# Performance work log

Hardware: AMD Instinct MI355X
Metric: run time of the kernel (lower is better)

## Reference

```python
import jax, jax.numpy as jnp
import numpy as np

V, B, T, D, H = 32000, 64, 256, 512, 1024


def setup_inputs() -> dict:
    key = jax.random.key(0)
    ks = jax.random.split(key, 8)
    s = lambda i, shape: (jax.random.normal(ks[i], shape, jnp.float32) * 0.02)
    return {
        "y": jax.random.randint(ks[0], (B, T), 0, V),
        "hidden": jnp.zeros((B, H), jnp.float32),
        "emb_table": s(1, (V, D)),
        "Wx": s(2, (D, 3 * H)),
        "Wh": s(3, (H, 3 * H)),
        "bx": jnp.zeros((3 * H,), jnp.float32),
        "bh": jnp.zeros((3 * H,), jnp.float32),
        "W_out": s(4, (H, D)),
        "b_out": jnp.zeros((D,), jnp.float32),
    }


def _gru_step(h, x, Wx, Wh, bx, bh):
    # PyTorch GRUCell semantics: r,z gates, candidate n with r gating the
    # recurrent contribution (including its bias term).
    gx = x @ Wx + bx          # [B, 3H]
    gh = h @ Wh + bh          # [B, 3H]
    xr, xz, xn = jnp.split(gx, 3, axis=-1)
    hr, hz, hn = jnp.split(gh, 3, axis=-1)
    r = jax.nn.sigmoid(xr + hr)
    z = jax.nn.sigmoid(xz + hz)
    n = jnp.tanh(xn + r * hn)
    return (1.0 - z) * n + z * h


def reference(y, hidden, emb_table, Wx, Wh, bx, bh, W_out, b_out):
    emb = emb_table[y]                       # [B, T, D] token embedding lookup

    def step(h, x_t):                        # x_t: [B, D]
        h2 = _gru_step(h, x_t, Wx, Wh, bx, bh)
        return h2, h2

    _, outs = jax.lax.scan(step, hidden, jnp.swapaxes(emb, 0, 1))  # [T, B, H]
    out = jnp.swapaxes(outs, 0, 1)           # [B, T, H] decoder hiddens
    logits = jnp.tanh(out @ W_out + b_out)   # [B, T, D]; dropout_rate=0 -> identity
    return logits
```

## Files before the change

kernel.cpp:

```cpp
#include <hip/hip_runtime.h>
#include <stdint.h>

typedef unsigned short u16;
typedef unsigned int u32;
typedef __attribute__((ext_vector_type(4))) unsigned int u32x4;
typedef __attribute__((ext_vector_type(4))) float f32x4;
typedef __attribute__((ext_vector_type(8))) __bf16 bf16x8;

#define MFMA16(a, b, c) __builtin_amdgcn_mfma_f32_16x16x32_bf16((a), (b), (c), 0, 0, 0)

__device__ __forceinline__ u16 f2b(float f) {
  union { float f; unsigned u; } v; v.f = f;
  unsigned r = v.u + 0x7FFFu + ((v.u >> 16) & 1u);
  return (u16)(r >> 16);
}
__device__ __forceinline__ float b2f(u16 h) {
  union { unsigned u; float f; } v; v.u = ((unsigned)h) << 16;
  return v.f;
}
__device__ __forceinline__ float sigm(float x) { return 1.0f / (1.0f + __expf(-x)); }
__device__ __forceinline__ float tanh_fast(float x) {
  x = fminf(fmaxf(x, -15.0f), 15.0f);
  float t = __expf(2.0f * x);
  return (t - 1.0f) / (t + 1.0f);
}

__device__ __forceinline__ void st16_sc(void* p, u32x4 v) {
  asm volatile("global_store_dwordx4 %0, %1, off sc0 sc1"
               :: "v"(p), "v"(v) : "memory");
}
__device__ __forceinline__ void st4_sc(u32* p, u32 v) {
  asm volatile("global_store_dword %0, %1, off sc0 sc1"
               :: "v"(p), "v"(v) : "memory");
}


__global__ void transpose_cvt(const float* __restrict__ src, u16* __restrict__ dst,
                              int R, int C) {
  __shared__ float tile[32][33];
  const int c0 = blockIdx.x * 32, r0 = blockIdx.y * 32;
  const int tx = threadIdx.x, ty = threadIdx.y;
  for (int i = ty; i < 32; i += 8)
    tile[i][tx] = src[(size_t)(r0 + i) * C + (c0 + tx)];
  __syncthreads();
  for (int i = ty; i < 32; i += 8)
    dst[(size_t)(c0 + i) * R + (r0 + tx)] = f2b(tile[tx][i]);
}

__global__ void gather_cast(const int* __restrict__ y, const float* __restrict__ tab,
                            u16* __restrict__ A) {
  const int idx = blockIdx.x * 256 + threadIdx.x;
  const int m = idx >> 7;
  const int d0 = (idx & 127) << 2;
  const float4 v = *reinterpret_cast<const float4*>(tab + (size_t)y[m] * 512 + d0);
  ushort4 o;
  o.x = f2b(v.x); o.y = f2b(v.y); o.z = f2b(v.z); o.w = f2b(v.w);
  *reinterpret_cast<ushort4*>(A + (size_t)m * 512 + d0) = o;
}

__global__ void cast_h0_blocked(const float* __restrict__ h, u16* __restrict__ dst) {
  const int i = blockIdx.x * 256 + threadIdx.x;
  const int b = i >> 10, n = i & 1023;
  const int r = b >> 4, ii = b & 15, g = n >> 4, j = n & 15;
  dst[((size_t)r * 64 + g) * 256 + ii * 16 + j] = f2b(h[(size_t)b * 1024 + n]);
}

template <int EPI, int ALAYOUT>
__global__ __launch_bounds__(256, 2) void gemm_bt(
    const u16* __restrict__ A, const u16* __restrict__ Bt,
    const float* __restrict__ bias, void* __restrict__ Cout,
    int M, int N, int K) {
  __shared__ u16 As[4096], Bs[4096];
  const int tid = threadIdx.x, lane = tid & 63, w = tid >> 6;
  const int wm = w >> 1, wn = w & 1, c = lane & 15, hq = lane >> 4;
  const int m0 = blockIdx.y * 128, n0 = blockIdx.x * 128;
  f32x4 acc[4][4] = {};

  const int slot0 = tid, slot1 = 256 + tid;
  const int r0_ = slot0 >> 2, ko0 = (slot0 & 3) << 3;
  const int r1_ = slot1 >> 2, ko1 = (slot1 & 3) << 3;

  for (int k0 = 0; k0 < K; k0 += 32) {
    u32x4 a0, a1;
    if (ALAYOUT == 0) {
      a0 = *(const u32x4*)(A + (size_t)(m0 + r0_) * K + k0 + ko0);
      a1 = *(const u32x4*)(A + (size_t)(m0 + r1_) * K + k0 + ko1);
    } else {
      const int ma = m0 + r0_, ka = k0 + ko0, mb = m0 + r1_, kb = k0 + ko1;
      a0 = *(const u32x4*)(A + ((((size_t)(ma >> 6) + 1) * 4 + ((ma >> 4) & 3)) * 64 +
                                (ka >> 4)) * 256 + (ma & 15) * 16 + (ka & 15));
      a1 = *(const u32x4*)(A + ((((size_t)(mb >> 6) + 1) * 4 + ((mb >> 4) & 3)) * 64 +
                                (kb >> 4)) * 256 + (mb & 15) * 16 + (kb & 15));
    }
    const u32x4 b0 = *(const u32x4*)(Bt + (size_t)(n0 + r0_) * K + k0 + ko0);
    const u32x4 b1 = *(const u32x4*)(Bt + (size_t)(n0 + r1_) * K + k0 + ko1);
    __syncthreads();
    *(u32x4*)(As + r0_ * 32 + ko0) = a0;
    *(u32x4*)(As + r1_ * 32 + ko1) = a1;
    *(u32x4*)(Bs + r0_ * 32 + ko0) = b0;
    *(u32x4*)(Bs + r1_ * 32 + ko1) = b1;
    __syncthreads();
    u32x4 af[4], bf[4];
#pragma unroll
    for (int i = 0; i < 4; ++i) {
      af[i] = *(const u32x4*)(As + (wm * 64 + i * 16 + c) * 32 + hq * 8);
      bf[i] = *(const u32x4*)(Bs + (wn * 64 + i * 16 + c) * 32 + hq * 8);
    }
#pragma unroll
    for (int mi = 0; mi < 4; ++mi)
#pragma unroll
      for (int ni = 0; ni < 4; ++ni)
        acc[mi][ni] = MFMA16(__builtin_bit_cast(bf16x8, af[mi]),
                             __builtin_bit_cast(bf16x8, bf[ni]), acc[mi][ni]);
  }

#pragma unroll
  for (int ni = 0; ni < 4; ++ni) {
    const int col = n0 + wn * 64 + ni * 16 + c;
    const float bv = bias[col];
#pragma unroll
    for (int mi = 0; mi < 4; ++mi) {
#pragma unroll
      for (int i = 0; i < 4; ++i) {
        const int m = m0 + wm * 64 + mi * 16 + hq * 4 + i;
        const float v = acc[mi][ni][i] + bv;
        if (EPI == 0) {
          const int dr = (m & 255) * 64 + (m >> 8);
          ((u16*)Cout)[(size_t)dr * N + col] = f2b(v);
        } else {
          const int dr = (m & 63) * 256 + (m >> 6);
          ((float*)Cout)[(size_t)dr * N + col] = tanh_fast(v);
        }
      }
    }
  }
}

__global__ __launch_bounds__(320, 1) void scan_kernel(
    const u16* __restrict__ wh_t,
    const float* __restrict__ bh,
    const float* __restrict__ h0,
    const u16* __restrict__ gx,
    u16* __restrict__ hbuf,
    u32* __restrict__ tags) {
  __shared__ u16 whs[96 * 512];
  __shared__ float red[2][4][3][256];
  __shared__ __align__(16) u16 htile[16][16];
  const int g = blockIdx.x >> 2, r = blockIdx.x & 3;
  const int tid = threadIdx.x, lane = tid & 63, s = tid >> 6;
  const int c = lane & 15, hq = lane >> 4;
  const int gcol = g * 16 + c;
  const int row0 = r * 16;

  for (int fb = s; fb < 96; fb += 5) {
    const int ss = fb / 24, kk = (fb % 24) / 3, ct = fb % 3;
    const int n = ct * 1024 + g * 16 + c;
    const int k = ss * 256 + kk * 32 + hq * 8;
    *(u32x4*)(whs + fb * 512 + lane * 8) =
        *(const u32x4*)(wh_t + (size_t)n * 1024 + k);
  }
  float bhv[3], hprev[4];
  u16 gxr[4][3];
  if (s == 4) {
#pragma unroll
    for (int ct = 0; ct < 3; ++ct) bhv[ct] = bh[ct * 1024 + gcol];
#pragma unroll
    for (int i = 0; i < 4; ++i)
      hprev[i] = h0[(size_t)(row0 + hq * 4 + i) * 1024 + gcol];
    const u16* gp = gx + gcol;
#pragma unroll
    for (int i = 0; i < 4; ++i) {
      const int b = row0 + hq * 4 + i;
      gxr[i][0] = gp[(size_t)b * 3072];
      gxr[i][1] = gp[(size_t)b * 3072 + 1024];
      gxr[i][2] = gp[(size_t)b * 3072 + 2048];
    }
  }
  __syncthreads();

  for (int t = 0; t < 256; ++t) {
    if (s < 4) {
      if (t > 0) {
        const u32* tp = tags + ((size_t)(t & 1) * 4 + r) * (64 * 32) +
                        (s * 16 + (lane & 15)) * 32;
        u32 v0, v1;
        asm volatile("global_load_dword %0, %1, off sc0 sc1" : "=v"(v0) : "v"(tp));
        asm volatile("global_load_dword %0, %1, off sc0 sc1" : "=v"(v1) : "v"(tp));
        while (true) {
          asm volatile("s_waitcnt vmcnt(1)" ::: "memory");
          if (!__ballot(v0 < (u32)t)) break;
          asm volatile("global_load_dword %0, %1, off sc0 sc1" : "=v"(v0) : "v"(tp));
          asm volatile("s_waitcnt vmcnt(1)" ::: "memory");
          if (!__ballot(v1 < (u32)t)) break;
          asm volatile("global_load_dword %0, %1, off sc0 sc1" : "=v"(v1) : "v"(tp));
        }
        asm volatile("s_waitcnt vmcnt(0)" ::: "memory");
      }

      u32x4 af[8];
      {
        const u16* ap0 = hbuf + ((size_t)t * 4 + r) * 16384 +
                         (s * 16 + (hq >> 1)) * 256 + c * 16 + (hq & 1) * 8;
        const u16* ap1 = ap0 + 2048;
        af[0] = *(const u32x4*)(ap0);
        af[1] = *(const u32x4*)(ap0 + 512);
        af[2] = *(const u32x4*)(ap0 + 1024);
        af[3] = *(const u32x4*)(ap0 + 1536);
        af[4] = *(const u32x4*)(ap1);
        af[5] = *(const u32x4*)(ap1 + 512);
        af[6] = *(const u32x4*)(ap1 + 1024);
        af[7] = *(const u32x4*)(ap1 + 1536);
      }

      f32x4 acc[3] = {};
#pragma unroll
      for (int kk = 0; kk < 8; ++kk) {
        const int fb = (s * 8 + kk) * 3;
        const u32x4 b0 = *(const u32x4*)(whs + (fb + 0) * 512 + lane * 8);
        const u32x4 b1 = *(const u32x4*)(whs + (fb + 1) * 512 + lane * 8);
        const u32x4 b2 = *(const u32x4*)(whs + (fb + 2) * 512 + lane * 8);
        const bf16x8 a = __builtin_bit_cast(bf16x8, af[kk]);
        acc[0] = MFMA16(a, __builtin_bit_cast(bf16x8, b0), acc[0]);
        acc[1] = MFMA16(a, __builtin_bit_cast(bf16x8, b1), acc[1]);
        acc[2] = MFMA16(a, __builtin_bit_cast(bf16x8, b2), acc[2]);
      }
#pragma unroll
      for (int ct = 0; ct < 3; ++ct)
        *(f32x4*)&red[t & 1][s][ct][lane * 4] = acc[ct];
    }
    __syncthreads();

    if (s == 4) {
      f32x4 a0 = {}, a1 = {}, a2 = {};
#pragma unroll
      for (int j = 0; j < 4; ++j) {
        a0 += *(const f32x4*)&red[t & 1][j][0][lane * 4];
        a1 += *(const f32x4*)&red[t & 1][j][1][lane * 4];
        a2 += *(const f32x4*)&red[t & 1][j][2][lane * 4];
      }
#pragma unroll
      for (int i = 0; i < 4; ++i) {
        const float xr = b2f(gxr[i][0]);
        const float xz = b2f(gxr[i][1]);
        const float xn = b2f(gxr[i][2]);
        const float rr = sigm(xr + a0[i] + bhv[0]);
        const float zz = sigm(xz + a1[i] + bhv[1]);
        const float nn = tanh_fast(xn + rr * (a2[i] + bhv[2]));
        const float hnew = (1.0f - zz) * nn + zz * hprev[i];
        hprev[i] = hnew;
        htile[hq * 4 + i][c] = f2b(hnew);
      }
      asm volatile("s_waitcnt lgkmcnt(0)" ::: "memory");
      __builtin_amdgcn_sched_barrier(0);
      if (lane < 32) {
        const u32x4 hv = *(const u32x4*)((const u16*)htile + lane * 8);
        st16_sc(hbuf + ((size_t)(t + 1) * 4 + r) * 16384 + g * 256 + lane * 8, hv);
      }
      asm volatile("s_waitcnt vmcnt(0)" ::: "memory");
      if (lane == 0)
        st4_sc(tags + ((size_t)((t + 1) & 1) * 4 + r) * (64 * 32) + g * 32,
               (u32)(t + 1));
      if (t < 255) {
        const u16* gp = gx + (size_t)(t + 1) * 64 * 3072 + gcol;
#pragma unroll
        for (int i = 0; i < 4; ++i) {
          const int b = row0 + hq * 4 + i;
          gxr[i][0] = gp[(size_t)b * 3072];
          gxr[i][1] = gp[(size_t)b * 3072 + 1024];
          gxr[i][2] = gp[(size_t)b * 3072 + 2048];
        }
      }
    }
  }
}

extern "C" void kernel_launch(void* const* d_in, const int* in_sizes, int n_in,
                              void* d_out, int out_size, void* d_ws, size_t ws_size,
                              hipStream_t stream) {
  (void)in_sizes; (void)n_in; (void)out_size; (void)ws_size;
  const int* y = (const int*)d_in[0];
  const float* hidden = (const float*)d_in[1];
  const float* emb = (const float*)d_in[2];
  const float* Wx = (const float*)d_in[3];
  const float* Wh = (const float*)d_in[4];
  const float* bx = (const float*)d_in[5];
  const float* bh = (const float*)d_in[6];
  const float* Wout = (const float*)d_in[7];
  const float* bout = (const float*)d_in[8];

  char* p = (char*)d_ws;
  u16* wx_t = (u16*)p; p += (size_t)3072 * 512 * 2;
  u16* wh_t = (u16*)p; p += (size_t)3072 * 1024 * 2;
  u16* wo_t = (u16*)p; p += (size_t)512 * 1024 * 2;
  u16* aemb = (u16*)p; p += (size_t)16384 * 512 * 2;
  u16* gx   = (u16*)p; p += (size_t)16384 * 3072 * 2;
  u16* hbuf = (u16*)p; p += (size_t)257 * 4 * 64 * 256 * 2;
  u32* tags = (u32*)p;

  hipMemsetAsync(tags, 0, 2 * 4 * 64 * 32 * sizeof(u32), stream);
  transpose_cvt<<<dim3(96, 16), dim3(32, 8), 0, stream>>>(Wx, wx_t, 512, 3072);
  transpose_cvt<<<dim3(96, 32), dim3(32, 8), 0, stream>>>(Wh, wh_t, 1024, 3072);
  transpose_cvt<<<dim3(16, 32), dim3(32, 8), 0, stream>>>(Wout, wo_t, 1024, 512);
  gather_cast<<<dim3(8192), dim3(256), 0, stream>>>(y, emb, aemb);
  cast_h0_blocked<<<dim3(256), dim3(256), 0, stream>>>(hidden, hbuf);

  gemm_bt<0, 0><<<dim3(24, 128), dim3(256), 0, stream>>>(aemb, wx_t, bx, (void*)gx,
                                                         16384, 3072, 512);
  scan_kernel<<<dim3(256), dim3(320), 0, stream>>>(wh_t, bh, hidden, gx,
                                                   hbuf, tags);
  gemm_bt<1, 1><<<dim3(4, 128), dim3(256), 0, stream>>>(hbuf, wo_t, bout,
                                                        d_out, 16384, 512, 1024);
}
```

Measured before the change: 1.057 ms.

## Restructure GRU scan: one block per column group, each wave owns a batch slice

Before, each of 256 blocks (one column group crossed with one batch quarter) split K across four waves and reduced the partial sums in shared memory, with a fifth wave doing the gate math. Now 64 blocks each cover one column group, and each of four waves owns 16 batch rows and does the full K=1024 reduction in registers with 32 MFMA steps. That removes the shared-memory reduction, the __syncthreads and the separate epilogue wave. Hidden-state loads use staged vmcnt waits to overlap the loads with the MFMAs. The cost is 4x fewer blocks and a longer serial MFMA chain per wave each step, and each wave now polls all 64 tags for its batch slice.

```diff
diff --git a/kernel.cpp b/kernel.cpp
--- a/kernel.cpp
+++ b/kernel.cpp
@@ -25,6 +25,13 @@
   return (t - 1.0f) / (t + 1.0f);
 }
 
+template <int OFF>
+__device__ __forceinline__ u32x4 ld16_sc(const void* p) {
+  u32x4 r;
+  asm volatile("global_load_dwordx4 %0, %1, off offset:%2 sc0 sc1"
+               : "=v"(r) : "v"(p), "i"(OFF));
+  return r;
+}
 __device__ __forceinline__ void st16_sc(void* p, u32x4 v) {
   asm volatile("global_store_dwordx4 %0, %1, off sc0 sc1"
                :: "v"(p), "v"(v) : "memory");
@@ -32,6 +39,13 @@
 __device__ __forceinline__ void st4_sc(u32* p, u32 v) {
   asm volatile("global_store_dword %0, %1, off sc0 sc1"
                :: "v"(p), "v"(v) : "memory");
+}
+__device__ __forceinline__ u32 ld4_sc(const u32* p) {
+  u32 r;
+  asm volatile("global_load_dword %0, %1, off sc0 sc1\n\t"
+               "s_waitcnt vmcnt(0)"
+               : "=v"(r) : "v"(p) : "memory");
+  return r;
 }
 
 
@@ -61,8 +75,8 @@
 __global__ void cast_h0_blocked(const float* __restrict__ h, u16* __restrict__ dst) {
   const int i = blockIdx.x * 256 + threadIdx.x;
   const int b = i >> 10, n = i & 1023;
-  const int r = b >> 4, ii = b & 15, g = n >> 4, j = n & 15;
-  dst[((size_t)r * 64 + g) * 256 + ii * 16 + j] = f2b(h[(size_t)b * 1024 + n]);
+  const int w = b >> 4, ii = b & 15, g = n >> 4, j = n & 15;
+  dst[((size_t)w * 64 + g) * 256 + ii * 16 + j] = f2b(h[(size_t)b * 1024 + n]);
 }
 
 template <int EPI, int ALAYOUT>
@@ -136,7 +150,7 @@
   }
 }
 
-__global__ __launch_bounds__(320, 1) void scan_kernel(
+__global__ __launch_bounds__(256, 1) void scan_kernel(
     const u16* __restrict__ wh_t,
     const float* __restrict__ bh,
     const float* __restrict__ h0,
@@ -144,29 +158,28 @@
     u16* __restrict__ hbuf,
     u32* __restrict__ tags) {
   __shared__ u16 whs[96 * 512];
-  __shared__ float red[2][4][3][256];
-  __shared__ __align__(16) u16 htile[16][16];
-  const int g = blockIdx.x >> 2, r = blockIdx.x & 3;
-  const int tid = threadIdx.x, lane = tid & 63, s = tid >> 6;
+  __shared__ __align__(16) u16 htile[4][256];
+  const int g = blockIdx.x;
+  const int tid = threadIdx.x, lane = tid & 63, w = tid >> 6;
   const int c = lane & 15, hq = lane >> 4;
   const int gcol = g * 16 + c;
-  const int row0 = r * 16;
-
-  for (int fb = s; fb < 96; fb += 5) {
-    const int ss = fb / 24, kk = (fb % 24) / 3, ct = fb % 3;
+  const int row0 = w * 16;
+
+  for (int fb = w; fb < 96; fb += 4) {
+    const int kk = fb / 3, ct = fb % 3;
     const int n = ct * 1024 + g * 16 + c;
-    const int k = ss * 256 + kk * 32 + hq * 8;
+    const int k = kk * 32 + hq * 8;
     *(u32x4*)(whs + fb * 512 + lane * 8) =
         *(const u32x4*)(wh_t + (size_t)n * 1024 + k);
   }
   float bhv[3], hprev[4];
   u16 gxr[4][3];
-  if (s == 4) {
-#pragma unroll
-    for (int ct = 0; ct < 3; ++ct) bhv[ct] = bh[ct * 1024 + gcol];
-#pragma unroll
-    for (int i = 0; i < 4; ++i)
-      hprev[i] = h0[(size_t)(row0 + hq * 4 + i) * 1024 + gcol];
+#pragma unroll
+  for (int ct = 0; ct < 3; ++ct) bhv[ct] = bh[ct * 1024 + gcol];
+#pragma unroll
+  for (int i = 0; i < 4; ++i)
+    hprev[i] = h0[(size_t)(row0 + hq * 4 + i) * 1024 + gcol];
+  {
     const u16* gp = gx + gcol;
 #pragma unroll
     for (int i = 0; i < 4; ++i) {
@@ -179,98 +192,80 @@
   __syncthreads();
 
   for (int t = 0; t < 256; ++t) {
-    if (s < 4) {
-      if (t > 0) {
-        const u32* tp = tags + ((size_t)(t & 1) * 4 + r) * (64 * 32) +
-                        (s * 16 + (lane & 15)) * 32;
-        u32 v0, v1;
-        asm volatile("global_load_dword %0, %1, off sc0 sc1" : "=v"(v0) : "v"(tp));
-        asm volatile("global_load_dword %0, %1, off sc0 sc1" : "=v"(v1) : "v"(tp));
-        while (true) {
-          asm volatile("s_waitcnt vmcnt(1)" ::: "memory");
-          if (!__ballot(v0 < (u32)t)) break;
-          asm volatile("global_load_dword %0, %1, off sc0 sc1" : "=v"(v0) : "v"(tp));
-          asm volatile("s_waitcnt vmcnt(1)" ::: "memory");
-          if (!__ballot(v1 < (u32)t)) break;
-          asm volatile("global_load_dword %0, %1, off sc0 sc1" : "=v"(v1) : "v"(tp));
-        }
-        asm volatile("s_waitcnt vmcnt(0)" ::: "memory");
+    if (t > 0) {
+      const u32* tp = tags + ((size_t)(t & 1) * 4 + w) * (64 * 32) + lane * 32;
+      while (__ballot(ld4_sc(tp) < (u32)t)) {}
+    }
+
+    u32x4 af[32];
+    {
+      const u16* bs = hbuf + ((size_t)t * 4 + w) * 16384 +
+                      (hq >> 1) * 256 + c * 16 + (hq & 1) * 8;
+#pragma unroll
+      for (int j = 0; j < 8; ++j) {
+        const u16* ap = bs + j * 2048;
+        af[j * 4 + 0] = ld16_sc<0>(ap);
+        af[j * 4 + 1] = ld16_sc<1024>(ap);
+        af[j * 4 + 2] = ld16_sc<2048>(ap);
+        af[j * 4 + 3] = ld16_sc<3072>(ap);
       }
-
-      u32x4 af[8];
-      {
-        const u16* ap0 = hbuf + ((size_t)t * 4 + r) * 16384 +
-                         (s * 16 + (hq >> 1)) * 256 + c * 16 + (hq & 1) * 8;
-        const u16* ap1 = ap0 + 2048;
-        af[0] = *(const u32x4*)(ap0);
-        af[1] = *(const u32x4*)(ap0 + 512);
-        af[2] = *(const u32x4*)(ap0 + 1024);
-        af[3] = *(const u32x4*)(ap0 + 1536);
-        af[4] = *(const u32x4*)(ap1);
-        af[5] = *(const u32x4*)(ap1 + 512);
-        af[6] = *(const u32x4*)(ap1 + 1024);
-        af[7] = *(const u32x4*)(ap1 + 1536);
-      }
-
-      f32x4 acc[3] = {};
-#pragma unroll
-      for (int kk = 0; kk < 8; ++kk) {
-        const int fb = (s * 8 + kk) * 3;
-        const u32x4 b0 = *(const u32x4*)(whs + (fb + 0) * 512 + lane * 8);
-        const u32x4 b1 = *(const u32x4*)(whs + (fb + 1) * 512 + lane * 8);
-        const u32x4 b2 = *(const u32x4*)(whs + (fb + 2) * 512 + lane * 8);
+    }
+
+    f32x4 acc[3] = {};
+#pragma unroll
+    for (int ph = 0; ph < 4; ++ph) {
+      if (ph == 0)      asm volatile("s_waitcnt vmcnt(24)" ::: "memory");
+      else if (ph == 1) asm volatile("s_waitcnt vmcnt(16)" ::: "memory");
+      else if (ph == 2) asm volatile("s_waitcnt vmcnt(8)" ::: "memory");
+      else              asm volatile("s_waitcnt vmcnt(0)" ::: "memory");
+      __builtin_amdgcn_sched_barrier(0);
+#pragma unroll
+      for (int q = 0; q < 8; ++q) {
+        const int kk = ph * 8 + q;
         const bf16x8 a = __builtin_bit_cast(bf16x8, af[kk]);
+        const u32x4 b0 = *(const u32x4*)(whs + (kk * 3 + 0) * 512 + lane * 8);
+        const u32x4 b1 = *(const u32x4*)(whs + (kk * 3 + 1) * 512 + lane * 8);
+        const u32x4 b2 = *(const u32x4*)(whs + (kk * 3 + 2) * 512 + lane * 8);
         acc[0] = MFMA16(a, __builtin_bit_cast(bf16x8, b0), acc[0]);
         acc[1] = MFMA16(a, __builtin_bit_cast(bf16x8, b1), acc[1]);
         acc[2] = MFMA16(a, __builtin_bit_cast(bf16x8, b2), acc[2]);
       }
-#pragma unroll
-      for (int ct = 0; ct < 3; ++ct)
-        *(f32x4*)&red[t & 1][s][ct][lane * 4] = acc[ct];
-    }
-    __syncthreads();
-
-    if (s == 4) {
-      f32x4 a0 = {}, a1 = {}, a2 = {};
-#pragma unroll
-      for (int j = 0; j < 4; ++j) {
-        a0 += *(const f32x4*)&red[t & 1][j][0][lane * 4];
-        a1 += *(const f32x4*)&red[t & 1][j][1][lane * 4];
-        a2 += *(const f32x4*)&red[t & 1][j][2][lane * 4];
+    }
+
+#pragma unroll
+    for (int i = 0; i < 4; ++i) {
+      const float xr = b2f(gxr[i][0]);
+      const float xz = b2f(gxr[i][1]);
+      const float xn = b2f(gxr[i][2]);
+      const float rr = sigm(xr + acc[0][i] + bhv[0]);
+      const float zz = sigm(xz + acc[1][i] + bhv[1]);
+      const float nn = tanh_fast(xn + rr * (acc[2][i] + bhv[2]));
+      const float hnew = (1.0f - zz) * nn + zz * hprev[i];
+      hprev[i] = hnew;
+      htile[w][(hq * 4 + i) * 16 + c] = f2b(hnew);
+    }
+
+    if (t < 255) {
+      const u16* gp = gx + (size_t)(t + 1) * 64 * 3072 + gcol;
+#pragma unroll
+      for (int i = 0; i < 4; ++i) {
+        const int b = row0 + hq * 4 + i;
+        gxr[i][0] = gp[(size_t)b * 3072];
+        gxr[i][1] = gp[(size_t)b * 3072 + 1024];
+        gxr[i][2] = gp[(size_t)b * 3072 + 2048];
       }
-#pragma unroll
-      for (int i = 0; i < 4; ++i) {
-        const float xr = b2f(gxr[i][0]);
-        const float xz = b2f(gxr[i][1]);
-        const float xn = b2f(gxr[i][2]);
-        const float rr = sigm(xr + a0[i] + bhv[0]);
-        const float zz = sigm(xz + a1[i] + bhv[1]);
-        const float nn = tanh_fast(xn + rr * (a2[i] + bhv[2]));
-        const float hnew = (1.0f - zz) * nn + zz * hprev[i];
-        hprev[i] = hnew;
-        htile[hq * 4 + i][c] = f2b(hnew);
-      }
-      asm volatile("s_waitcnt lgkmcnt(0)" ::: "memory");
-      __builtin_amdgcn_sched_barrier(0);
-      if (lane < 32) {
-        const u32x4 hv = *(const u32x4*)((const u16*)htile + lane * 8);
-        st16_sc(hbuf + ((size_t)(t + 1) * 4 + r) * 16384 + g * 256 + lane * 8, hv);
-      }
-      asm volatile("s_waitcnt vmcnt(0)" ::: "memory");
-      if (lane == 0)
-        st4_sc(tags + ((size_t)((t + 1) & 1) * 4 + r) * (64 * 32) + g * 32,
-               (u32)(t + 1));
-      if (t < 255) {
-        const u16* gp = gx + (size_t)(t + 1) * 64 * 3072 + gcol;
-#pragma unroll
-        for (int i = 0; i < 4; ++i) {
-          const int b = row0 + hq * 4 + i;
-          gxr[i][0] = gp[(size_t)b * 3072];
-          gxr[i][1] = gp[(size_t)b * 3072 + 1024];
-          gxr[i][2] = gp[(size_t)b * 3072 + 2048];
-        }
-      }
-    }
+    }
+
+    asm volatile("s_waitcnt lgkmcnt(0)" ::: "memory");
+    __builtin_amdgcn_sched_barrier(0);
+    if (lane < 32) {
+      const u32x4 hv = *(const u32x4*)(&htile[w][lane * 8]);
+      st16_sc(hbuf + ((size_t)(t + 1) * 4 + w) * 16384 + g * 256 + lane * 8, hv);
+    }
+    asm volatile("s_waitcnt vmcnt(0)" ::: "memory");
+    if (lane == 0)
+      st4_sc(tags + ((size_t)((t + 1) & 1) * 4 + w) * (64 * 32) + g * 32,
+             (u32)(t + 1));
   }
 }
 
@@ -306,8 +301,8 @@
 
   gemm_bt<0, 0><<<dim3(24, 128), dim3(256), 0, stream>>>(aemb, wx_t, bx, (void*)gx,
                                                          16384, 3072, 512);
-  scan_kernel<<<dim3(256), dim3(320), 0, stream>>>(wh_t, bh, hidden, gx,
-                                                   hbuf, tags);
+  scan_kernel<<<dim3(64), dim3(256), 0, stream>>>(wh_t, bh, hidden, gx,
+                                                  hbuf, tags);
   gemm_bt<1, 1><<<dim3(4, 128), dim3(256), 0, stream>>>(hbuf, wo_t, bout,
                                                         d_out, 16384, 512, 1024);
 }
```

Result: slower. 1.360 ms (+28.7%).
